# Performance work log

Measured on AMD Instinct MI355X. Metric: run time of the kernel, lower is better.

Reference implementation:

```python
import jax, jax.numpy as jnp
import numpy as np

NUM_BINS = 256
WS = 5          # ssim_window_size
SIGMA = 1.5
LEVELS = 5
MS_WEIGHTS = jnp.asarray(np.array([0.0448, 0.2856, 0.3001, 0.2363, 0.1333], dtype=np.float32))


def _gauss_window():
    x = np.arange(WS) - WS // 2
    g = np.exp(-(x.astype(np.float64) ** 2) / (2.0 * SIGMA ** 2))
    g = g / g.sum()
    return jnp.asarray(np.outer(g, g), dtype=jnp.float32)  # (WS, WS)


def _conv_same(x, w):
    # x: (H, W), w: (WS, WS); 'SAME' pad == torch padding=WS//2 for odd WS
    return jax.lax.conv_general_dilated(x[None, None], w[None, None], (1, 1), 'SAME')[0, 0]


def _rgb_to_lab(img):
    # img: (3, H, W) in [0,1] -> normalized LAB (3, H, W)  (CURL ImageProcessing.rgb_to_lab)
    H, W = img.shape[1], img.shape[2]
    x = jnp.transpose(img, (2, 1, 0)).reshape(-1, 3)  # (W*H, 3)
    lin = jnp.where(x <= 0.04045, x / 12.92,
                    ((jnp.maximum(x, 1e-4) + 0.055) / 1.055) ** 2.4)
    rgb2xyz = jnp.array([[0.412453, 0.212671, 0.019334],
                         [0.357580, 0.715160, 0.119193],
                         [0.180423, 0.072169, 0.950227]], dtype=img.dtype)
    xyz = lin @ rgb2xyz
    xyz = xyz * jnp.array([1.0 / 0.950456, 1.0, 1.0 / 1.088754], dtype=img.dtype)
    eps = 6.0 / 29.0
    f = jnp.where(xyz <= eps ** 3,
                  xyz / (3.0 * eps ** 2) + 4.0 / 29.0,
                  jnp.maximum(xyz, 1e-4) ** (1.0 / 3.0))
    f2lab = jnp.array([[0.0, 500.0, 0.0],
                       [116.0, -500.0, 200.0],
                       [0.0, 0.0, -200.0]], dtype=img.dtype)
    lab = f @ f2lab + jnp.array([-16.0, 0.0, 0.0], dtype=img.dtype)
    lab = jnp.transpose(lab.reshape(W, H, 3), (2, 1, 0))  # (3, H, W)
    return jnp.stack([lab[0] / 100.0,
                      (lab[1] / 110.0 + 1.0) / 2.0,
                      (lab[2] / 110.0 + 1.0) / 2.0])


def _histogram(img):
    # img: (3, H, W) in [0,1] -> per-channel 256-bin count histogram (3, NUM_BINS)
    idx = jnp.clip(jnp.floor(img * NUM_BINS).astype(jnp.int32), 0, NUM_BINS - 1)
    per_ch = lambda ix: jnp.zeros((NUM_BINS,), jnp.float32).at[ix.reshape(-1)].add(1.0)
    return jax.vmap(per_ch)(idx)


def _ssim(i1, i2, w):
    # i1, i2: (H, W) single-channel images
    mu1 = _conv_same(i1, w)
    mu2 = _conv_same(i2, w)
    s1 = _conv_same(i1 * i1, w) - mu1 * mu1
    s2 = _conv_same(i2 * i2, w) - mu2 * mu2
    s12 = _conv_same(i1 * i2, w) - mu1 * mu2
    C1, C2 = 0.01 ** 2, 0.03 ** 2
    ssim_map = ((2.0 * mu1 * mu2 + C1) * (2.0 * s12 + C2)) / \
               ((mu1 * mu1 + mu2 * mu2 + C1) * (s1 + s2 + C2))
    cs = jnp.mean((2.0 * s12 + C2) / (s1 + s2 + C2))
    return ssim_map.mean(), cs


def _avg_pool2(x):
    H, W = x.shape
    return x.reshape(H // 2, 2, W // 2, 2).mean(axis=(1, 3))


def _msssim(i1, i2, w):
    mssim, mcs = [], []
    for _ in range(LEVELS):
        s, cs = _ssim(i1, i2, w)
        mssim.append(s)
        mcs.append(cs)
        i1 = _avg_pool2(i1)
        i2 = _avg_pool2(i2)
    mssim = (jnp.stack(mssim) + 1.0) / 2.0
    mcs = (jnp.stack(mcs) + 1.0) / 2.0
    return jnp.prod(mcs[:LEVELS - 1] ** MS_WEIGHTS[:LEVELS - 1]) * mssim[LEVELS - 1] ** MS_WEIGHTS[LEVELS - 1]


def _forward(input_image_batch, predicted_img_batch, target_img_batch):
    pred_lab = jnp.clip(jax.vmap(_rgb_to_lab)(predicted_img_batch), 0.0, 1.0)
    tgt_lab = jnp.clip(jax.vmap(_rgb_to_lab)(target_img_batch), 0.0, 1.0)

    # histogram loss: original loop does h_i = (h_{i-1} + l1_i + 1) / 2; closed form below
    hp = jax.vmap(_histogram)(pred_lab)   # (B, 3, NUM_BINS)
    ht = jax.vmap(_histogram)(tgt_lab)
    l1_hist = jnp.mean(jnp.abs(hp - ht), axis=(1, 2))  # (B,)
    n = l1_hist.shape[0]
    wgt = 2.0 ** (jnp.arange(n, dtype=jnp.float32) - n)  # 2^{-(n-i)}
    hist_loss = jnp.sum(wgt * (l1_hist + 1.0))

    # MS-SSIM on L channel, per image (is_identity=True -> no variational_prediction)
    window = _gauss_window()
    ms = jax.vmap(lambda a, b: _msssim(a, b, window))(pred_lab[:, 0], tgt_lab[:, 0])
    ssim_loss = jnp.mean(1.0 - ms)

    lab_l1 = jnp.mean(jnp.abs(pred_lab - tgt_lab))  # mean of per-image means (same-size imgs)

    H, W = input_image_batch.shape[2], input_image_batch.shape[3]
    scaler = H * W / 20.0
    hist_loss = hist_loss / n / scaler
    lab_loss = lab_l1 + hist_loss
    return lab_loss.reshape(1, 1), ssim_loss.reshape(1, 1)


def setup_inputs():
    key = jax.random.key(0)
    k1, k2, k3 = jax.random.split(key, 3)
    B, C, H, W = 8, 3, 512, 512
    return {
        'input_image_batch': jax.random.uniform(k1, (B, C, H, W), jnp.float32),
        'predicted_img_batch': jax.random.uniform(k2, (B, C, H, W), jnp.float32),
        'target_img_batch': jax.random.uniform(k3, (B, C, H, W), jnp.float32),
        'is_identity': 1,
    }


def reference(input_image_batch, predicted_img_batch, target_img_batch, is_identity):
    return _forward(input_image_batch, predicted_img_batch, target_img_batch)
```

## Files before the change

### kernel.cpp

```cpp
#include <hip/hip_runtime.h>
#include <math.h>

#define B 8
#define IMH 512
#define IMW 512
#define HW (IMH*IMW)
#define NBINS 256

#define PYR_PER_IMG (65536 + 16384 + 4096 + 1024)
#define PYR_OFF_L1 0
#define PYR_OFF_L2 65536
#define PYR_OFF_L3 81920
#define PYR_OFF_L4 86016

#define OFF_PPYR 0
#define OFF_TPYR (B*PYR_PER_IMG)
#define OFF_HISTPART (2*B*PYR_PER_IMG)
#define OFF_LABPART  (OFF_HISTPART + B*256*768)
#define OFF_CSP      (OFF_LABPART + B*256)
#define OFF_LVLS     (OFF_CSP + B*256)
#define OFF_LVLC     (OFF_LVLS + B*85)
#define OFF_HISTL1   (OFF_LVLC + B*85)

typedef float f2 __attribute__((ext_vector_type(2)));

__device__ __forceinline__ f2 mkf2(float a, float b) { f2 r; r.x = a; r.y = b; return r; }
__device__ __forceinline__ f2 shfl_down_f2(f2 v, int d) {
    return mkf2(__shfl_down(v.x, d, 64), __shfl_down(v.y, d, 64));
}
__device__ __forceinline__ f2 shfl_f2(f2 v, int src) {
    return mkf2(__shfl(v.x, src, 64), __shfl(v.y, src, 64));
}
__device__ __forceinline__ f2 clamp01_f2(f2 a) {
    a.x = fminf(fmaxf(a.x, 0.0f), 1.0f);
    a.y = fminf(fmaxf(a.y, 0.0f), 1.0f);
    return a;
}

__device__ __forceinline__ float fastpow(float x, float y) {
    return __builtin_amdgcn_exp2f(y * __builtin_amdgcn_logf(x));
}

__device__ __forceinline__ void rgb2lab_pk(f2 r, f2 g, f2 b, f2 lab[3]) {
    f2 v[3] = {r, g, b};
    f2 lin[3];
    #pragma unroll
    for (int c = 0; c < 3; ++c) {
        f2 x = v[c];
        float hx = fastpow((fmaxf(x.x, 1e-4f) + 0.055f) * (float)(1.0/1.055), 2.4f);
        float hy = fastpow((fmaxf(x.y, 1e-4f) + 0.055f) * (float)(1.0/1.055), 2.4f);
        lin[c].x = (x.x <= 0.04045f) ? x.x * (float)(1.0/12.92) : hx;
        lin[c].y = (x.y <= 0.04045f) ? x.y * (float)(1.0/12.92) : hy;
    }
    f2 X = 0.412453f*lin[0] + 0.357580f*lin[1] + 0.180423f*lin[2];
    f2 Y = 0.212671f*lin[0] + 0.715160f*lin[1] + 0.072169f*lin[2];
    f2 Z = 0.019334f*lin[0] + 0.119193f*lin[1] + 0.950227f*lin[2];
    X = X * (float)(1.0/0.950456);
    Z = Z * (float)(1.0/1.088754);
    const float eps3   = (float)((6.0/29.0)*(6.0/29.0)*(6.0/29.0));
    const float rd3e2  = (float)(1.0/(3.0*(6.0/29.0)*(6.0/29.0)));
    const float c429   = (float)(4.0/29.0);
    f2 xyz[3] = {X, Y, Z};
    f2 f[3];
    #pragma unroll
    for (int c = 0; c < 3; ++c) {
        float ax = xyz[c].x, ay = xyz[c].y;
        f[c].x = (ax <= eps3) ? (ax * rd3e2 + c429) : fastpow(fmaxf(ax, 1e-4f), (float)(1.0/3.0));
        f[c].y = (ay <= eps3) ? (ay * rd3e2 + c429) : fastpow(fmaxf(ay, 1e-4f), (float)(1.0/3.0));
    }
    f2 L  = 116.0f*f[1] - 16.0f;
    f2 A  = 500.0f*f[0] - 500.0f*f[1];
    f2 Bc = 200.0f*f[1] - 200.0f*f[2];
    lab[0] = L * 0.01f;
    lab[1] = (A * (float)(1.0/110.0) + 1.0f) * 0.5f;
    lab[2] = (Bc * (float)(1.0/110.0) + 1.0f) * 0.5f;
}

#define TST 37

template<bool WANT_S>
__device__ __forceinline__ void conv_ssim(const f2* tile, int t, float& ssum, float& csum) {
    double gd[5]; double gs = 0.0;
    #pragma unroll
    for (int i = 0; i < 5; ++i) { gd[i] = exp(-(double)((i-2)*(i-2)) / 4.5); gs += gd[i]; }
    float gw[5];
    #pragma unroll
    for (int i = 0; i < 5; ++i) gw[i] = (float)(gd[i] / gs);

    int lx = t & 31;
    int yg = t >> 5;

    f2 rA[8], rB[8];
    float r12[8];
    #pragma unroll
    for (int k = 0; k < 8; ++k) {
        int row = yg * 4 + k;
        const f2* p = &tile[row * TST + lx];
        f2 sA = {0.f, 0.f}, sB = {0.f, 0.f};
        float s12 = 0.f;
        #pragma unroll
        for (int dx = 0; dx < 5; ++dx) {
            f2 av = p[dx];
            float wv = gw[dx];
            sA += wv * av;
            f2 sq = av * av;
            sB += wv * sq;
            s12 = fmaf(wv, av.x * av.y, s12);
        }
        rA[k] = sA; rB[k] = sB; r12[k] = s12;
    }

    const float C1 = (float)(0.01 * 0.01);
    const float C2 = (float)(0.03 * 0.03);
    if constexpr (WANT_S) ssum = 0.f;
    csum = 0.f;
    #pragma unroll
    for (int j = 0; j < 4; ++j) {
        f2 mA = {0.f, 0.f}, mB = {0.f, 0.f};
        float m12 = 0.f;
        #pragma unroll
        for (int k = 0; k < 5; ++k) {
            float wv = gw[k];
            mA += wv * rA[j + k];
            mB += wv * rB[j + k];
            m12 = fmaf(wv, r12[j + k], m12);
        }
        float m1 = mA.x, m2 = mA.y;
        float v1  = mB.x - m1 * m1;
        float v2  = mB.y - m2 * m2;
        float v12 = m12 - m1 * m2;
        float n12 = 2.0f * v12 + C2;
        float rd2 = __builtin_amdgcn_rcpf(v1 + v2 + C2);
        csum = fmaf(n12, rd2, csum);
        if constexpr (WANT_S) {
            float rd1 = __builtin_amdgcn_rcpf(m1*m1 + m2*m2 + C1);
            ssum += (2.0f*m1*m2 + C1) * n12 * rd1 * rd2;
        }
    }
}

__device__ __forceinline__ void halo_coords(int h, int& hr, int& hc) {
    if (h < 72)       { hr = h / 36;            hc = h % 36; }
    else if (h < 144) { int u = h - 72;  hr = 34 + u / 36; hc = u % 36; }
    else              { int u = h - 144; hr = 2 + (u >> 2); int q = u & 3; hc = (q < 2) ? q : 32 + q; }
}

__global__ void lab_ssim0_kernel(const float* __restrict__ pred,
                                 const float* __restrict__ tgt,
                                 unsigned* __restrict__ histPart,
                                 float* __restrict__ labPart,
                                 float* __restrict__ csPart,
                                 float* __restrict__ ppyr,
                                 float* __restrict__ tpyr) {
    __shared__ f2 ls[36 * TST];
    __shared__ unsigned lhist[6 * NBINS];
    __shared__ f2 s1[16 * 16];
    __shared__ float red12[12];

    int t  = threadIdx.x;
    int b  = blockIdx.y;
    int bx = blockIdx.x;

    int tile = ((bx & 7) << 5) | (bx >> 3);
    int tx0 = (tile & 15) << 5;
    int ty0 = (tile >> 4) << 5;
    int r   = t >> 3;
    int c4  = (t & 7) << 2;
    int gy  = ty0 + r;

    const float* pimg = pred + (size_t)b * 3 * HW;
    const float* timg = tgt  + (size_t)b * 3 * HW;
    size_t ibase = (size_t)gy * IMW + tx0 + c4;

    float prA[4], pgA[4], pbA[4], trA[4], tgA[4], tbA[4];
    *(float4*)&prA[0] = *(const float4*)(pimg + ibase);
    *(float4*)&pgA[0] = *(const float4*)(pimg + ibase + HW);
    *(float4*)&pbA[0] = *(const float4*)(pimg + ibase + 2*HW);
    *(float4*)&trA[0] = *(const float4*)(timg + ibase);
    *(float4*)&tgA[0] = *(const float4*)(timg + ibase + HW);
    *(float4*)&tbA[0] = *(const float4*)(timg + ibase + 2*HW);

    int hr0, hc0;
    halo_coords(t, hr0, hc0);
    int hy0 = ty0 - 2 + hr0;
    int hx0 = tx0 - 2 + hc0;
    bool hv0 = ((unsigned)hy0 < 512u) && ((unsigned)hx0 < 512u);
    size_t ho = hv0 ? ((size_t)hy0 * IMW + hx0) : 0;
    float h_pr = pimg[ho], h_pg = pimg[ho + HW], h_pb = pimg[ho + 2*HW];
    float h_tr = timg[ho], h_tg = timg[ho + HW], h_tb = timg[ho + 2*HW];

    for (int i = t; i < 6 * NBINS; i += 256) lhist[i] = 0;
    __syncthreads();

    float l1 = 0.0f;
    f2 pL[4];
    #pragma unroll
    for (int k = 0; k < 4; ++k) {
        f2 lab[3];
        rgb2lab_pk(mkf2(prA[k], trA[k]), mkf2(pgA[k], tgA[k]), mkf2(pbA[k], tbA[k]), lab);
        #pragma unroll
        for (int c = 0; c < 3; ++c) {
            f2 lc = clamp01_f2(lab[c]);
            l1 += fabsf(lc.x - lc.y);
            int ip = min(max((int)floorf(lc.x * (float)NBINS), 0), NBINS - 1);
            int it = min(max((int)floorf(lc.y * (float)NBINS), 0), NBINS - 1);
            atomicAdd(&lhist[c * NBINS + ip], 1u);
            atomicAdd(&lhist[(3 + c) * NBINS + it], 1u);
            if (c == 0) pL[k] = lc;
        }
    }
    {
        f2* dst = &ls[(r + 2) * TST + (c4 + 2)];
        dst[0] = pL[0]; dst[1] = pL[1]; dst[2] = pL[2]; dst[3] = pL[3];
    }

    {
        f2 lab[3];
        rgb2lab_pk(mkf2(h_pr, h_tr), mkf2(h_pg, h_tg), mkf2(h_pb, h_tb), lab);
        f2 Lv = hv0 ? clamp01_f2(lab[0]) : mkf2(0.f, 0.f);
        ls[hr0 * TST + hc0] = Lv;
    }
    if (t < 16) {
        int hr, hc;
        halo_coords(256 + t, hr, hc);
        int hy = ty0 - 2 + hr;
        int hx = tx0 - 2 + hc;
        f2 Lv = {0.f, 0.f};
        if ((unsigned)hy < 512u && (unsigned)hx < 512u) {
            size_t o = (size_t)hy * IMW + hx;
            f2 lab[3];
            rgb2lab_pk(mkf2(pimg[o], timg[o]),
                       mkf2(pimg[o + HW], timg[o + HW]),
                       mkf2(pimg[o + 2*HW], timg[o + 2*HW]), lab);
            Lv = clamp01_f2(lab[0]);
        }
        ls[hr * TST + hc] = Lv;
    }
    __syncthreads();

    unsigned* hp = histPart + ((size_t)b * 256 + bx) * 768;
    for (int i = t; i < 768; i += 256)
        hp[i] = (lhist[2*i] & 0xFFFFu) | (lhist[2*i + 1] << 16);

    float* pyrP = ppyr + (size_t)b * PYR_PER_IMG;
    float* pyrT = tpyr + (size_t)b * PYR_PER_IMG;
    f2 ph0 = pL[0] + pL[1], ph1 = pL[2] + pL[3];
    f2 ph0b = shfl_down_f2(ph0, 8);
    f2 ph1b = shfl_down_f2(ph1, 8);
    if ((t & 8) == 0) {
        int y1 = r >> 1;
        int x1 = (t & 7) << 1;
        f2 v0 = 0.25f * (ph0 + ph0b);
        f2 v1 = 0.25f * (ph1 + ph1b);
        s1[y1 * 16 + x1]     = v0;
        s1[y1 * 16 + x1 + 1] = v1;
        int g1 = ((ty0 >> 1) + y1) * 256 + (tx0 >> 1) + x1;
        *(float2*)&pyrP[PYR_OFF_L1 + g1] = make_float2(v0.x, v1.x);
        *(float2*)&pyrT[PYR_OFF_L1 + g1] = make_float2(v0.y, v1.y);
    }
    __syncthreads();

    float sdummy, csum;
    conv_ssim<false>(ls, t, sdummy, csum);

    if (t < 64) {
        int y2 = t >> 3, x2 = t & 7;
        const f2* s = &s1[(2*y2) * 16 + 2*x2];
        f2 v2 = 0.25f * (s[0] + s[1] + s[16] + s[17]);
        pyrP[PYR_OFF_L2 + ((ty0 >> 2) + y2) * 128 + (tx0 >> 2) + x2] = v2.x;
        pyrT[PYR_OFF_L2 + ((ty0 >> 2) + y2) * 128 + (tx0 >> 2) + x2] = v2.y;

        int y3 = (t >> 2) & 3, x3 = t & 3;
        f2 v3 = 0.25f * (shfl_f2(v2, (2*y3)*8 + 2*x3)     + shfl_f2(v2, (2*y3)*8 + 2*x3 + 1) +
                         shfl_f2(v2, (2*y3+1)*8 + 2*x3)   + shfl_f2(v2, (2*y3+1)*8 + 2*x3 + 1));
        if (t < 16) {
            pyrP[PYR_OFF_L3 + ((ty0 >> 3) + y3) * 64 + (tx0 >> 3) + x3] = v3.x;
            pyrT[PYR_OFF_L3 + ((ty0 >> 3) + y3) * 64 + (tx0 >> 3) + x3] = v3.y;
        }
        int y4 = (t >> 1) & 1, x4 = t & 1;
        f2 v4 = 0.25f * (shfl_f2(v3, (2*y4)*4 + 2*x4)     + shfl_f2(v3, (2*y4)*4 + 2*x4 + 1) +
                         shfl_f2(v3, (2*y4+1)*4 + 2*x4)   + shfl_f2(v3, (2*y4+1)*4 + 2*x4 + 1));
        if (t < 4) {
            pyrP[PYR_OFF_L4 + ((ty0 >> 4) + y4) * 32 + (tx0 >> 4) + x4] = v4.x;
            pyrT[PYR_OFF_L4 + ((ty0 >> 4) + y4) * 32 + (tx0 >> 4) + x4] = v4.y;
        }
    }

    int lane = t & 63;
    int wid  = t >> 6;
    #pragma unroll
    for (int o = 32; o >= 1; o >>= 1) {
        l1   += __shfl_down(l1, o, 64);
        csum += __shfl_down(csum, o, 64);
    }
    if (lane == 0) {
        red12[wid * 2 + 0] = l1;
        red12[wid * 2 + 1] = csum;
    }
    __syncthreads();
    if (t < 4) {
        float a0 = red12[t * 2 + 0];
        float a2 = red12[t * 2 + 1];
        #pragma unroll
        for (int o = 2; o >= 1; o >>= 1) {
            a0 += __shfl_down(a0, o, 64);
            a2 += __shfl_down(a2, o, 64);
        }
        if (t == 0) {
            labPart[b * 256 + bx] = a0;
            csPart[b * 256 + bx]  = a2;
        }
    }
}

__global__ void tail_kernel(const float* __restrict__ ppyr,
                            const float* __restrict__ tpyr,
                            const unsigned* __restrict__ histPart,
                            float* __restrict__ lvlS,
                            float* __restrict__ lvlC,
                            float* __restrict__ histL1p) {
    __shared__ f2 tls[36 * TST];
    __shared__ float red12[12];
    __shared__ int dLo[256];
    __shared__ int dHi[256];
    int t = threadIdx.x;
    int bx = blockIdx.x;

    if (bx < 48) {
        int b  = bx / 6;
        int w  = (bx % 6) * 64 + (t & 63);
        int ck = t >> 6;
        const unsigned* p = histPart + (size_t)b * 256 * 768 + (size_t)(ck * 64) * 768;
        unsigned sPlo = 0, sPhi = 0, sTlo = 0, sThi = 0;
        #pragma unroll 8
        for (int i = 0; i < 64; ++i) {
            unsigned wP = p[(size_t)i * 768 + w];
            unsigned wT = p[(size_t)i * 768 + 384 + w];
            sPlo += wP & 0xFFFFu;  sPhi += wP >> 16;
            sTlo += wT & 0xFFFFu;  sThi += wT >> 16;
        }
        dLo[t] = (int)sPlo - (int)sTlo;
        dHi[t] = (int)sPhi - (int)sThi;
        __syncthreads();
        if (t < 64) {
            int lo = dLo[t] + dLo[t + 64] + dLo[t + 128] + dLo[t + 192];
            int hi = dHi[t] + dHi[t + 64] + dHi[t + 128] + dHi[t + 192];
            float val = fabsf((float)lo) + fabsf((float)hi);
            #pragma unroll
            for (int o = 32; o >= 1; o >>= 1) val += __shfl_down(val, o, 64);
            if (t == 0) histL1p[bx] = val;
        }
    } else {
        int cb = bx - 48;
        int b = cb / 85;
        int sub = cb - b * 85;
        int lvl, pblk;
        if (sub < 64)      { lvl = 1; pblk = sub; }
        else if (sub < 80) { lvl = 2; pblk = sub - 64; }
        else if (sub < 84) { lvl = 3; pblk = sub - 80; }
        else               { lvl = 4; pblk = 0; }

        const int offs[5] = {0, PYR_OFF_L1, PYR_OFF_L2, PYR_OFF_L3, PYR_OFF_L4};
        int w = 512 >> lvl;
        const float* i1 = ppyr + (size_t)b * PYR_PER_IMG + offs[lvl];
        const float* i2 = tpyr + (size_t)b * PYR_PER_IMG + offs[lvl];

        int tprShift = 4 - lvl;
        int ty0 = (pblk >> tprShift) << 5;
        int tx0 = (pblk & ((1 << tprShift) - 1)) << 5;

        for (int i = t; i < 36 * 36; i += 256) {
            int r = i / 36, c = i % 36;
            int gy = ty0 - 2 + r;
            int gx = tx0 - 2 + c;
            bool ok = ((unsigned)gy < (unsigned)w) && ((unsigned)gx < (unsigned)w);
            int gi = gy * w + gx;
            tls[r * TST + c] = ok ? mkf2(i1[gi], i2[gi]) : mkf2(0.f, 0.f);
        }
        __syncthreads();

        float ssum, csum;
        conv_ssim<true>(tls, t, ssum, csum);

        int lane = t & 63;
        int wid  = t >> 6;
        #pragma unroll
        for (int o = 32; o >= 1; o >>= 1) {
            ssum += __shfl_down(ssum, o, 64);
            csum += __shfl_down(csum, o, 64);
        }
        if (lane == 0) {
            red12[wid * 2 + 0] = ssum;
            red12[wid * 2 + 1] = csum;
        }
        __syncthreads();
        if (t < 4) {
            float a1 = red12[t * 2 + 0];
            float a2 = red12[t * 2 + 1];
            #pragma unroll
            for (int o = 2; o >= 1; o >>= 1) {
                a1 += __shfl_down(a1, o, 64);
                a2 += __shfl_down(a2, o, 64);
            }
            if (t == 0) {
                lvlS[cb] = a1;
                lvlC[cb] = a2;
            }
        }
    }
}

__global__ void final_kernel(const float* __restrict__ labPart,
                             const float* __restrict__ csPart,
                             const float* __restrict__ lvlS,
                             const float* __restrict__ lvlC,
                             const float* __restrict__ histL1p,
                             float* __restrict__ out) {
    __shared__ double sh[48];
    __shared__ double wred[4];
    int t = threadIdx.x;

    {
        int b = t >> 5, k = t & 31;
        double s = 0.0;
        #pragma unroll
        for (int j = 0; j < 8; ++j) s += (double)csPart[b * 256 + k + 32 * j];
        #pragma unroll
        for (int o = 16; o >= 1; o >>= 1) s += __shfl_down(s, o, 32);
        if (k == 0) sh[b] = s;
    }
    {
        double s = 0.0;
        #pragma unroll
        for (int j = 0; j < 8; ++j) s += (double)labPart[t + 256 * j];
        #pragma unroll
        for (int o = 32; o >= 1; o >>= 1) s += __shfl_down(s, o, 64);
        if ((t & 63) == 0) wred[t >> 6] = s;
    }
    if (t < 32) {
        int b = t >> 2, q = t & 3;
        const int lo[4] = {0, 64, 80, 84};
        const int hi[4] = {64, 80, 84, 85};
        const float* src = (q == 3) ? lvlS : lvlC;
        double s = 0.0;
        for (int i = lo[q]; i < hi[q]; ++i) s += (double)src[b * 85 + i];
        sh[8 + q * 8 + b] = s;
    }
    if (t < 8) {
        double s = 0.0;
        #pragma unroll
        for (int j = 0; j < 6; ++j) s += (double)histL1p[t * 6 + j];
        sh[40 + t] = s;
    }
    __syncthreads();

    if (t < 8) {
        const float msw[5]  = {0.0448f, 0.2856f, 0.3001f, 0.2363f, 0.1333f};
        const float npix[5] = {(float)HW, (float)(HW/4), (float)(HW/16),
                               (float)(HW/64), (float)(HW/256)};
        int b = t;
        float l1 = (float)(sh[40 + b] / (double)(3 * NBINS));
        float wgt = __builtin_amdgcn_exp2f((float)(b - B));
        float histc = wgt * (l1 + 1.0f);
        float ms = 1.0f;
        float cs0 = (float)(sh[b] / (double)npix[0]);
        ms *= fastpow((cs0 + 1.0f) * 0.5f, msw[0]);
        #pragma unroll
        for (int l = 1; l <= 3; ++l) {
            float cs = (float)(sh[l * 8 + b] / (double)npix[l]);
            ms *= fastpow((cs + 1.0f) * 0.5f, msw[l]);
        }
        float sm = (float)(sh[32 + b] / (double)npix[4]);
        ms *= fastpow((sm + 1.0f) * 0.5f, msw[4]);
        float lossc = 1.0f - ms;
        #pragma unroll
        for (int o = 4; o >= 1; o >>= 1) {
            histc += __shfl_down(histc, o, 64);
            lossc += __shfl_down(lossc, o, 64);
        }
        if (t == 0) {
            double labSum = wred[0] + wred[1] + wred[2] + wred[3];
            float scaler = (float)HW / 20.0f;
            float hist_loss = histc / (float)B / scaler;
            float lab_l1 = (float)(labSum / (double)((size_t)B * 3 * HW));
            out[0] = lab_l1 + hist_loss;
            out[1] = lossc / (float)B;
        }
    }
}

extern "C" void kernel_launch(void* const* d_in, const int* in_sizes, int n_in,
                              void* d_out, int out_size, void* d_ws, size_t ws_size,
                              hipStream_t stream) {
    const float* pred = (const float*)d_in[1];
    const float* tgt  = (const float*)d_in[2];
    float* ws_f = (float*)d_ws;

    float* ppyr     = ws_f + OFF_PPYR;
    float* tpyr     = ws_f + OFF_TPYR;
    unsigned* histPart = (unsigned*)(ws_f + OFF_HISTPART);
    float* labPart  = ws_f + OFF_LABPART;
    float* csPart   = ws_f + OFF_CSP;
    float* lvlS     = ws_f + OFF_LVLS;
    float* lvlC     = ws_f + OFF_LVLC;
    float* histL1p  = ws_f + OFF_HISTL1;
    float* out = (float*)d_out;


    lab_ssim0_kernel<<<dim3(256, B), 256, 0, stream>>>(pred, tgt, histPart, labPart,
                                                       csPart, ppyr, tpyr);

    tail_kernel<<<728, 256, 0, stream>>>(ppyr, tpyr, histPart, lvlS, lvlC, histL1p);

    final_kernel<<<1, 256, 0, stream>>>(labPart, csPart, lvlS, lvlC, histL1p, out);
}
```

Before: 129.8 us.

## Process two vertically stacked tiles per block with prefetch of the second tile

Each block of the first kernel now handles two 32x32 tiles stacked vertically, which halves the grid to 128 blocks per image. The global loads for the second tile, including its halo, are issued before the first tile's convolution so their latency overlaps compute. The shared histogram is accumulated across both tiles and written once, which halves the histogram partials the tail and final kernels have to reduce. It also adds launch bounds of 256 threads with 4 blocks per CU, which raises register pressure from the prefetched data and leaves fewer blocks to hide latency.

Measured after the change: 181.0 us. 39.4% more time.

```diff
diff --git a/kernel.cpp b/kernel.cpp
--- a/kernel.cpp
+++ b/kernel.cpp
@@ -13,12 +13,14 @@
 #define PYR_OFF_L3 81920
 #define PYR_OFF_L4 86016
 
+#define NTILE 128
+
 #define OFF_PPYR 0
 #define OFF_TPYR (B*PYR_PER_IMG)
 #define OFF_HISTPART (2*B*PYR_PER_IMG)
-#define OFF_LABPART  (OFF_HISTPART + B*256*768)
-#define OFF_CSP      (OFF_LABPART + B*256)
-#define OFF_LVLS     (OFF_CSP + B*256)
+#define OFF_LABPART  (OFF_HISTPART + B*NTILE*768)
+#define OFF_CSP      (OFF_LABPART + B*NTILE)
+#define OFF_LVLS     (OFF_CSP + B*NTILE)
 #define OFF_LVLC     (OFF_LVLS + B*85)
 #define OFF_HISTL1   (OFF_LVLC + B*85)
 
@@ -145,59 +147,15 @@
     else              { int u = h - 144; hr = 2 + (u >> 2); int q = u & 3; hc = (q < 2) ? q : 32 + q; }
 }
 
-__global__ void lab_ssim0_kernel(const float* __restrict__ pred,
-                                 const float* __restrict__ tgt,
-                                 unsigned* __restrict__ histPart,
-                                 float* __restrict__ labPart,
-                                 float* __restrict__ csPart,
-                                 float* __restrict__ ppyr,
-                                 float* __restrict__ tpyr) {
-    __shared__ f2 ls[36 * TST];
-    __shared__ unsigned lhist[6 * NBINS];
-    __shared__ f2 s1[16 * 16];
-    __shared__ float red12[12];
-
-    int t  = threadIdx.x;
-    int b  = blockIdx.y;
-    int bx = blockIdx.x;
-
-    int tile = ((bx & 7) << 5) | (bx >> 3);
-    int tx0 = (tile & 15) << 5;
-    int ty0 = (tile >> 4) << 5;
-    int r   = t >> 3;
-    int c4  = (t & 7) << 2;
-    int gy  = ty0 + r;
-
-    const float* pimg = pred + (size_t)b * 3 * HW;
-    const float* timg = tgt  + (size_t)b * 3 * HW;
-    size_t ibase = (size_t)gy * IMW + tx0 + c4;
-
-    float prA[4], pgA[4], pbA[4], trA[4], tgA[4], tbA[4];
-    *(float4*)&prA[0] = *(const float4*)(pimg + ibase);
-    *(float4*)&pgA[0] = *(const float4*)(pimg + ibase + HW);
-    *(float4*)&pbA[0] = *(const float4*)(pimg + ibase + 2*HW);
-    *(float4*)&trA[0] = *(const float4*)(timg + ibase);
-    *(float4*)&tgA[0] = *(const float4*)(timg + ibase + HW);
-    *(float4*)&tbA[0] = *(const float4*)(timg + ibase + 2*HW);
-
-    int hr0, hc0;
-    halo_coords(t, hr0, hc0);
-    int hy0 = ty0 - 2 + hr0;
-    int hx0 = tx0 - 2 + hc0;
-    bool hv0 = ((unsigned)hy0 < 512u) && ((unsigned)hx0 < 512u);
-    size_t ho = hv0 ? ((size_t)hy0 * IMW + hx0) : 0;
-    float h_pr = pimg[ho], h_pg = pimg[ho + HW], h_pb = pimg[ho + 2*HW];
-    float h_tr = timg[ho], h_tg = timg[ho + HW], h_tb = timg[ho + 2*HW];
-
-    for (int i = t; i < 6 * NBINS; i += 256) lhist[i] = 0;
-    __syncthreads();
-
-    float l1 = 0.0f;
-    f2 pL[4];
+
+__device__ __forceinline__ void tile_interior(const float pr[4], const float pg[4], const float pb[4],
+                                              const float tr[4], const float tg[4], const float tb[4],
+                                              int r, int c4, f2* ls, unsigned* lhist,
+                                              float& l1, f2 pL[4]) {
     #pragma unroll
     for (int k = 0; k < 4; ++k) {
         f2 lab[3];
-        rgb2lab_pk(mkf2(prA[k], trA[k]), mkf2(pgA[k], tgA[k]), mkf2(pbA[k], tbA[k]), lab);
+        rgb2lab_pk(mkf2(pr[k], tr[k]), mkf2(pg[k], tg[k]), mkf2(pb[k], tb[k]), lab);
         #pragma unroll
         for (int c = 0; c < 3; ++c) {
             f2 lc = clamp01_f2(lab[c]);
@@ -209,17 +167,12 @@
             if (c == 0) pL[k] = lc;
         }
     }
-    {
-        f2* dst = &ls[(r + 2) * TST + (c4 + 2)];
-        dst[0] = pL[0]; dst[1] = pL[1]; dst[2] = pL[2]; dst[3] = pL[3];
-    }
-
-    {
-        f2 lab[3];
-        rgb2lab_pk(mkf2(h_pr, h_tr), mkf2(h_pg, h_tg), mkf2(h_pb, h_tb), lab);
-        f2 Lv = hv0 ? clamp01_f2(lab[0]) : mkf2(0.f, 0.f);
-        ls[hr0 * TST + hc0] = Lv;
-    }
+    f2* dst = &ls[(r + 2) * TST + (c4 + 2)];
+    dst[0] = pL[0]; dst[1] = pL[1]; dst[2] = pL[2]; dst[3] = pL[3];
+}
+
+__device__ __forceinline__ void tile_halo_rest(const float* pimg, const float* timg,
+                                               int t, int ty0, int tx0, f2* ls) {
     if (t < 16) {
         int hr, hc;
         halo_coords(256 + t, hr, hc);
@@ -236,14 +189,10 @@
         }
         ls[hr * TST + hc] = Lv;
     }
-    __syncthreads();
-
-    unsigned* hp = histPart + ((size_t)b * 256 + bx) * 768;
-    for (int i = t; i < 768; i += 256)
-        hp[i] = (lhist[2*i] & 0xFFFFu) | (lhist[2*i + 1] << 16);
-
-    float* pyrP = ppyr + (size_t)b * PYR_PER_IMG;
-    float* pyrT = tpyr + (size_t)b * PYR_PER_IMG;
+}
+
+__device__ __forceinline__ void tile_l1(const f2 pL[4], int t, int r, int ty0, int tx0,
+                                        f2* s1, float* pyrP, float* pyrT) {
     f2 ph0 = pL[0] + pL[1], ph1 = pL[2] + pL[3];
     f2 ph0b = shfl_down_f2(ph0, 8);
     f2 ph1b = shfl_down_f2(ph1, 8);
@@ -258,11 +207,10 @@
         *(float2*)&pyrP[PYR_OFF_L1 + g1] = make_float2(v0.x, v1.x);
         *(float2*)&pyrT[PYR_OFF_L1 + g1] = make_float2(v0.y, v1.y);
     }
-    __syncthreads();
-
-    float sdummy, csum;
-    conv_ssim<false>(ls, t, sdummy, csum);
-
+}
+
+__device__ __forceinline__ void tile_l24(int t, int ty0, int tx0, const f2* s1,
+                                         float* pyrP, float* pyrT) {
     if (t < 64) {
         int y2 = t >> 3, x2 = t & 7;
         const f2* s = &s1[(2*y2) * 16 + 2*x2];
@@ -285,6 +233,120 @@
             pyrT[PYR_OFF_L4 + ((ty0 >> 4) + y4) * 32 + (tx0 >> 4) + x4] = v4.y;
         }
     }
+}
+
+__global__ __launch_bounds__(256, 4)
+void lab_ssim0_kernel(const float* __restrict__ pred,
+                      const float* __restrict__ tgt,
+                      unsigned* __restrict__ histPart,
+                      float* __restrict__ labPart,
+                      float* __restrict__ csPart,
+                      float* __restrict__ ppyr,
+                      float* __restrict__ tpyr) {
+    __shared__ f2 ls[36 * TST];
+    __shared__ unsigned lhist[6 * NBINS];
+    __shared__ f2 s1[16 * 16];
+    __shared__ float red12[12];
+
+    int t  = threadIdx.x;
+    int b  = blockIdx.y;
+    int bx = blockIdx.x;
+
+    int tile = ((bx & 7) << 4) | (bx >> 3);
+    int tx0 = (tile & 15) << 5;
+    int ty0 = (tile >> 4) << 6;
+    int ty0B = ty0 + 32;
+    int r   = t >> 3;
+    int c4  = (t & 7) << 2;
+
+    const float* pimg = pred + (size_t)b * 3 * HW;
+    const float* timg = tgt  + (size_t)b * 3 * HW;
+    size_t ibase = (size_t)(ty0 + r) * IMW + tx0 + c4;
+
+    float prA[4], pgA[4], pbA[4], trA[4], tgA[4], tbA[4];
+    *(float4*)&prA[0] = *(const float4*)(pimg + ibase);
+    *(float4*)&pgA[0] = *(const float4*)(pimg + ibase + HW);
+    *(float4*)&pbA[0] = *(const float4*)(pimg + ibase + 2*HW);
+    *(float4*)&trA[0] = *(const float4*)(timg + ibase);
+    *(float4*)&tgA[0] = *(const float4*)(timg + ibase + HW);
+    *(float4*)&tbA[0] = *(const float4*)(timg + ibase + 2*HW);
+
+    int hr0, hc0;
+    halo_coords(t, hr0, hc0);
+    int hx0 = tx0 - 2 + hc0;
+    bool hxok = (unsigned)hx0 < 512u;
+    int hy0 = ty0 - 2 + hr0;
+    bool hvA = ((unsigned)hy0 < 512u) && hxok;
+    size_t hoA = hvA ? ((size_t)hy0 * IMW + hx0) : 0;
+    float haPr = pimg[hoA], haPg = pimg[hoA + HW], haPb = pimg[hoA + 2*HW];
+    float haTr = timg[hoA], haTg = timg[hoA + HW], haTb = timg[hoA + 2*HW];
+
+    for (int i = t; i < 6 * NBINS; i += 256) lhist[i] = 0;
+    __syncthreads();
+
+    float l1 = 0.0f;
+    float csum = 0.0f;
+    float* pyrP = ppyr + (size_t)b * PYR_PER_IMG;
+    float* pyrT = tpyr + (size_t)b * PYR_PER_IMG;
+
+    f2 pL[4];
+    tile_interior(prA, pgA, pbA, trA, tgA, tbA, r, c4, ls, lhist, l1, pL);
+
+    size_t ibaseB = ibase + (size_t)32 * IMW;
+    float prB[4], pgB[4], pbB[4], trB[4], tgB[4], tbB[4];
+    *(float4*)&prB[0] = *(const float4*)(pimg + ibaseB);
+    *(float4*)&pgB[0] = *(const float4*)(pimg + ibaseB + HW);
+    *(float4*)&pbB[0] = *(const float4*)(pimg + ibaseB + 2*HW);
+    *(float4*)&trB[0] = *(const float4*)(timg + ibaseB);
+    *(float4*)&tgB[0] = *(const float4*)(timg + ibaseB + HW);
+    *(float4*)&tbB[0] = *(const float4*)(timg + ibaseB + 2*HW);
+
+    int hy0B = ty0B - 2 + hr0;
+    bool hvB = ((unsigned)hy0B < 512u) && hxok;
+    size_t hoB = hvB ? ((size_t)hy0B * IMW + hx0) : 0;
+    float hbPr = pimg[hoB], hbPg = pimg[hoB + HW], hbPb = pimg[hoB + 2*HW];
+    float hbTr = timg[hoB], hbTg = timg[hoB + HW], hbTb = timg[hoB + 2*HW];
+
+    {
+        f2 lab[3];
+        rgb2lab_pk(mkf2(haPr, haTr), mkf2(haPg, haTg), mkf2(haPb, haTb), lab);
+        f2 Lv = hvA ? clamp01_f2(lab[0]) : mkf2(0.f, 0.f);
+        ls[hr0 * TST + hc0] = Lv;
+    }
+    tile_halo_rest(pimg, timg, t, ty0, tx0, ls);
+    tile_l1(pL, t, r, ty0, tx0, s1, pyrP, pyrT);
+    __syncthreads();
+
+    {
+        float sdummy, cs1;
+        conv_ssim<false>(ls, t, sdummy, cs1);
+        csum += cs1;
+    }
+    tile_l24(t, ty0, tx0, s1, pyrP, pyrT);
+    __syncthreads();
+
+    f2 pL2[4];
+    tile_interior(prB, pgB, pbB, trB, tgB, tbB, r, c4, ls, lhist, l1, pL2);
+    {
+        f2 lab[3];
+        rgb2lab_pk(mkf2(hbPr, hbTr), mkf2(hbPg, hbTg), mkf2(hbPb, hbTb), lab);
+        f2 Lv = hvB ? clamp01_f2(lab[0]) : mkf2(0.f, 0.f);
+        ls[hr0 * TST + hc0] = Lv;
+    }
+    tile_halo_rest(pimg, timg, t, ty0B, tx0, ls);
+    tile_l1(pL2, t, r, ty0B, tx0, s1, pyrP, pyrT);
+    __syncthreads();
+
+    unsigned* hp = histPart + ((size_t)b * NTILE + bx) * 768;
+    for (int i = t; i < 768; i += 256)
+        hp[i] = (lhist[2*i] & 0xFFFFu) | (lhist[2*i + 1] << 16);
+
+    {
+        float sdummy, cs2;
+        conv_ssim<false>(ls, t, sdummy, cs2);
+        csum += cs2;
+    }
+    tile_l24(t, ty0B, tx0, s1, pyrP, pyrT);
 
     int lane = t & 63;
     int wid  = t >> 6;
@@ -307,8 +369,8 @@
             a2 += __shfl_down(a2, o, 64);
         }
         if (t == 0) {
-            labPart[b * 256 + bx] = a0;
-            csPart[b * 256 + bx]  = a2;
+            labPart[b * NTILE + bx] = a0;
+            csPart[b * NTILE + bx]  = a2;
         }
     }
 }
@@ -330,10 +392,10 @@
         int b  = bx / 6;
         int w  = (bx % 6) * 64 + (t & 63);
         int ck = t >> 6;
-        const unsigned* p = histPart + (size_t)b * 256 * 768 + (size_t)(ck * 64) * 768;
+        const unsigned* p = histPart + (size_t)b * NTILE * 768 + (size_t)(ck * 32) * 768;
         unsigned sPlo = 0, sPhi = 0, sTlo = 0, sThi = 0;
         #pragma unroll 8
-        for (int i = 0; i < 64; ++i) {
+        for (int i = 0; i < 32; ++i) {
             unsigned wP = p[(size_t)i * 768 + w];
             unsigned wT = p[(size_t)i * 768 + 384 + w];
             sPlo += wP & 0xFFFFu;  sPhi += wP >> 16;
@@ -424,7 +486,7 @@
         int b = t >> 5, k = t & 31;
         double s = 0.0;
         #pragma unroll
-        for (int j = 0; j < 8; ++j) s += (double)csPart[b * 256 + k + 32 * j];
+        for (int j = 0; j < 4; ++j) s += (double)csPart[b * NTILE + k + 32 * j];
         #pragma unroll
         for (int o = 16; o >= 1; o >>= 1) s += __shfl_down(s, o, 32);
         if (k == 0) sh[b] = s;
@@ -432,7 +494,7 @@
     {
         double s = 0.0;
         #pragma unroll
-        for (int j = 0; j < 8; ++j) s += (double)labPart[t + 256 * j];
+        for (int j = 0; j < 4; ++j) s += (double)labPart[t + 256 * j];
         #pragma unroll
         for (int o = 32; o >= 1; o >>= 1) s += __shfl_down(s, o, 64);
         if ((t & 63) == 0) wred[t >> 6] = s;
@@ -507,8 +569,8 @@
     float* out = (float*)d_out;
 
 
-    lab_ssim0_kernel<<<dim3(256, B), 256, 0, stream>>>(pred, tgt, histPart, labPart,
-                                                       csPart, ppyr, tpyr);
+    lab_ssim0_kernel<<<dim3(NTILE, B), 256, 0, stream>>>(pred, tgt, histPart, labPart,
+                                                         csPart, ppyr, tpyr);
 
     tail_kernel<<<728, 256, 0, stream>>>(ppyr, tpyr, histPart, lvlS, lvlC, histL1p);
 
```
